# Kernel tuning notes

Hardware: AMD Instinct MI355X
Metric: run time of the kernel (lower is better)

The kernel has to match this reference:

```python
import jax, jax.numpy as jnp
import numpy as np

B, N, M, C, S = 4, 16384, 128, 128, 512  # batch, points, boxes, feat dim, sampled pts


def setup_inputs() -> dict:
    key = jax.random.key(0)
    k1, k2, k3, k4, k5, k6, k7 = jax.random.split(key, 7)
    # point cloud roughly in a LiDAR extent
    xy = jax.random.uniform(k1, (B, N, 2), minval=-50.0, maxval=50.0)
    z = jax.random.uniform(k2, (B, N, 1), minval=-3.0, maxval=3.0)
    points = jnp.concatenate([xy, z], axis=-1).astype(jnp.float32)
    point_features = jax.random.normal(k3, (B, N, C), dtype=jnp.float32)
    # boxes: (cx, cy, cz_bottom, dx, dy, dz, rz)
    ctr_xy = jax.random.uniform(k4, (B, M, 2), minval=-50.0, maxval=50.0)
    ctr_z = jax.random.uniform(k5, (B, M, 1), minval=-3.0, maxval=0.0)
    sizes = jax.random.uniform(k6, (B, M, 3), minval=2.0, maxval=8.0)
    rz = jax.random.uniform(k7, (B, M, 1), minval=-np.pi, maxval=np.pi)
    boxes3d = jnp.concatenate([ctr_xy, ctr_z, sizes, rz], axis=-1).astype(jnp.float32)
    return {"points": points, "point_features": point_features, "boxes3d": boxes3d}


def _pool_one_box(points, feats, box):
    # points (N,3), feats (N,C), box (7,)
    n = points.shape[0]
    cx, cy, cz, dx, dy, dz, rz = box
    cz = cz + 0.5 * dz  # bottom center -> geometric center (mmcv convention)
    sx = points[:, 0] - cx
    sy = points[:, 1] - cy
    cosa = jnp.cos(-rz)
    sina = jnp.sin(-rz)
    lx = sx * cosa - sy * sina
    ly = sx * sina + sy * cosa
    mask = (
        (jnp.abs(points[:, 2] - cz) <= 0.5 * dz)
        & (lx > -0.5 * dx) & (lx < 0.5 * dx)
        & (ly > -0.5 * dy) & (ly < 0.5 * dy)
    )
    cnt = mask.sum(dtype=jnp.int32)
    # rank of each in-box point among in-box points (first-come order)
    rank = jnp.cumsum(mask.astype(jnp.int32)) - 1
    pos = jnp.where(mask, rank, n)  # out-of-range for non-members -> dropped
    table = jnp.zeros((n,), jnp.int32).at[pos].set(
        jnp.arange(n, dtype=jnp.int32), mode="drop")
    # wrap-around duplication when cnt < S (kernel copies k % cnt)
    j = jnp.arange(S, dtype=jnp.int32) % jnp.maximum(cnt, 1)
    idx = table[j]  # (S,)
    pooled = jnp.concatenate([points[idx], feats[idx]], axis=-1)  # (S, 3+C)
    pooled = jnp.where(cnt > 0, pooled, jnp.zeros_like(pooled))
    empty = (cnt == 0).astype(jnp.int32)
    return pooled, empty


def reference(points, point_features, boxes3d):
    # vmap over boxes, then over batch
    per_scene = jax.vmap(_pool_one_box, in_axes=(None, None, 0))
    per_batch = jax.vmap(per_scene, in_axes=(0, 0, 0))
    pooled_features, pooled_empty_flag = per_batch(points, point_features, boxes3d)
    return pooled_features, pooled_empty_flag
```

## Files before the change

### kernel.cpp

```cpp
#include <hip/hip_runtime.h>

#define B_ 4
#define N_ 16384
#define M_ 128
#define C_ 128
#define S_ 512
#define ROW_ 131
#define NCHUNK_ 256
#define TILE_ 128
#define LSTR_ 136
#define KBOX_ 4

typedef float f4_t __attribute__((ext_vector_type(4)));

__device__ __forceinline__ int swz(int j, int col) {
    return j * LSTR_ + (col & 3) * 34 + (col >> 2);
}

__global__ __launch_bounds__(256) void mask_kernel(
    const float* __restrict__ points,
    const float* __restrict__ boxes,
    unsigned long long* __restrict__ masks,
    int* __restrict__ cnts)
{
    const int gwave = blockIdx.x * 4 + (threadIdx.x >> 6);
    const int lane  = threadIdx.x & 63;
    const int grp   = gwave >> 4;
    const int seg   = gwave & 15;
    const int bm0   = grp * KBOX_;
    const int b     = bm0 >> 7;

    const float* pb = points + (size_t)b * N_ * 3;
    float px[16], py[16], pz[16];
    #pragma unroll
    for (int k = 0; k < 16; ++k) {
        const int i = (seg * 16 + k) * 64 + lane;
        px[k] = pb[i*3+0]; py[k] = pb[i*3+1]; pz[k] = pb[i*3+2];
    }

    for (int kb = 0; kb < KBOX_; ++kb) {
        const int bm = bm0 + kb;
        const float* bx = boxes + bm * 7;
        const float cx = bx[0], cy = bx[1], czb = bx[2];
        const float dx = bx[3], dy = bx[4], dzv = bx[5], rz = bx[6];
        const float cz   = __fadd_rn(czb, __fmul_rn(0.5f, dzv));
        const float cosa = (float)cos(-(double)rz);
        const float sina = (float)sin(-(double)rz);
        const float hdx = 0.5f * dx, hdy = 0.5f * dy, hdz = 0.5f * dzv;

        #pragma unroll
        for (int k = 0; k < 16; ++k) {
            const float sx = __fsub_rn(px[k], cx);
            const float sy = __fsub_rn(py[k], cy);
            const float lx = __fsub_rn(__fmul_rn(sx, cosa), __fmul_rn(sy, sina));
            const float ly = __fadd_rn(__fmul_rn(sx, sina), __fmul_rn(sy, cosa));
            const bool pred = (fabsf(__fsub_rn(pz[k], cz)) <= hdz) &&
                              (lx > -hdx) && (lx < hdx) &&
                              (ly > -hdy) && (ly < hdy);
            const unsigned long long m = __ballot(pred);
            if (lane == 0) {
                const int chunk = seg * 16 + k;
                masks[(size_t)bm * NCHUNK_ + chunk] = m;
                cnts [(size_t)bm * NCHUNK_ + chunk] = __popcll(m);
            }
        }
    }
}

__global__ __launch_bounds__(256) void pool_kernel(
    const float* __restrict__ points,
    const float* __restrict__ feats,
    const unsigned long long* __restrict__ masks,
    const int* __restrict__ cnts,
    float* __restrict__ out,
    float* __restrict__ flags_out)
{
    const int bm  = blockIdx.x;
    const int b   = bm >> 7;
    const int tid = threadIdx.x;

    __shared__ int   sc[NCHUNK_];
    __shared__ int   s_idx[S_];
    __shared__ int   jtab[S_ + 1];
    __shared__ float srow[TILE_ * LSTR_];

    const int c = cnts[(size_t)bm * NCHUNK_ + tid];
    sc[tid] = c;
    __syncthreads();
    for (int off = 1; off < NCHUNK_; off <<= 1) {
        const int v = (tid >= off) ? sc[tid - off] : 0;
        __syncthreads();
        sc[tid] += v;
        __syncthreads();
    }
    const int total = sc[NCHUNK_ - 1];
    const int P = sc[tid] - c;

    if (c > 0 && P < S_) {
        unsigned long long m = masks[(size_t)bm * NCHUNK_ + tid];
        int pos = P;
        while (m && pos < S_) {
            const int bit = __ffsll((unsigned long long)m) - 1;
            m &= m - 1;
            s_idx[pos++] = tid * 64 + bit;
        }
    }
    __syncthreads();

    const int cnt_eff = total < S_ ? total : S_;
    const int denom   = cnt_eff > 0 ? cnt_eff : 1;
    for (int s = tid; s <= S_; s += 256) jtab[s] = (s < S_) ? (s % denom) : 0;

    const int T = cnt_eff < TILE_ ? cnt_eff : TILE_;
    if (total == 0) {
        if (tid < LSTR_) srow[tid] = 0.0f;
    } else {
        const int nf4 = T * 32;
        for (int t = tid; t < nf4; t += 256) {
            const int u = t >> 5, q = t & 31;
            const size_t pbase = (size_t)b * N_ + (unsigned)s_idx[u];
            const f4_t v = *(const f4_t*)(feats + pbase * C_ + q * 4);
            #pragma unroll
            for (int jj = 0; jj < 4; ++jj)
                srow[swz(u, 3 + 4 * q + jj)] = v[jj];
        }
        for (int t = tid; t < T * 3; t += 256) {
            const int u = t / 3, k = t - u * 3;
            const size_t pbase = (size_t)b * N_ + (unsigned)s_idx[u];
            srow[swz(u, k)] = points[pbase * 3 + k];
        }
    }
    __syncthreads();

    float* ob = out + (size_t)bm * (S_ * ROW_);
    for (int f = tid; f < (S_ * ROW_) / 4; f += 256) {
        const int e = 4 * f;
        const unsigned s0 = (unsigned)e / (unsigned)ROW_;
        const int col0 = e - (int)s0 * ROW_;
        const int ja = jtab[s0], jb = jtab[s0 + 1];
        f4_t v;
        if ((ja < TILE_) & (jb < TILE_)) {
            #pragma unroll
            for (int jj = 0; jj < 4; ++jj) {
                int col = col0 + jj;
                const bool cross = col >= ROW_;
                col = cross ? col - ROW_ : col;
                const int j = cross ? jb : ja;
                v[jj] = srow[swz(j, col)];
            }
        } else {
            #pragma unroll
            for (int jj = 0; jj < 4; ++jj) {
                int col = col0 + jj;
                unsigned s = s0;
                if (col >= ROW_) { col -= ROW_; ++s; }
                const int j = jtab[s];
                float val;
                if (j < TILE_) {
                    val = srow[swz(j, col)];
                } else {
                    const size_t pbase = (size_t)b * N_ + (unsigned)s_idx[j];
                    val = (col < 3) ? points[pbase * 3 + col]
                                    : feats[pbase * C_ + (col - 3)];
                }
                v[jj] = val;
            }
        }
        __builtin_nontemporal_store(v, (f4_t*)(ob + e));
    }
    if (tid == 0) flags_out[bm] = (total == 0) ? 1.0f : 0.0f;
}

extern "C" void kernel_launch(void* const* d_in, const int* in_sizes, int n_in,
                              void* d_out, int out_size, void* d_ws, size_t ws_size,
                              hipStream_t stream) {
    const float* points = (const float*)d_in[0];
    const float* feats  = (const float*)d_in[1];
    const float* boxes  = (const float*)d_in[2];
    float* out = (float*)d_out;

    unsigned long long* masks = (unsigned long long*)d_ws;
    int* cnts = (int*)((char*)d_ws + (size_t)B_ * M_ * NCHUNK_ * 8);

    float* flags = out + (size_t)B_ * M_ * S_ * ROW_;

    mask_kernel<<<B_ * M_ * 16 / 4 / KBOX_, 256, 0, stream>>>(
        points, boxes, masks, cnts);
    pool_kernel<<<B_ * M_, 256, 0, stream>>>(points, feats, masks, cnts, out, flags);
}
```

Before: 187.2 us.

## Fuse point-in-box mask computation into pooling kernel, keep masks in LDS

Merges the separate mask kernel into the pool kernel. Each block computes its own box's in-box ballot masks and per-chunk counts over all 16384 points, writes them to shared memory, then runs the scan and gather as before. This removes a kernel launch and the global round trip for masks and counts. In exchange, each block now scans the full point array by itself with only 512 blocks of 4 waves, which could lengthen the serial mask phase before the bandwidth-heavy output writes.

```diff
diff --git a/kernel.cpp b/kernel.cpp
--- a/kernel.cpp
+++ b/kernel.cpp
@@ -9,7 +9,6 @@
 #define NCHUNK_ 256
 #define TILE_ 128
 #define LSTR_ 136
-#define KBOX_ 4
 
 typedef float f4_t __attribute__((ext_vector_type(4)));
 
@@ -17,76 +16,55 @@
     return j * LSTR_ + (col & 3) * 34 + (col >> 2);
 }
 
-__global__ __launch_bounds__(256) void mask_kernel(
-    const float* __restrict__ points,
-    const float* __restrict__ boxes,
-    unsigned long long* __restrict__ masks,
-    int* __restrict__ cnts)
-{
-    const int gwave = blockIdx.x * 4 + (threadIdx.x >> 6);
-    const int lane  = threadIdx.x & 63;
-    const int grp   = gwave >> 4;
-    const int seg   = gwave & 15;
-    const int bm0   = grp * KBOX_;
-    const int b     = bm0 >> 7;
-
-    const float* pb = points + (size_t)b * N_ * 3;
-    float px[16], py[16], pz[16];
-    #pragma unroll
-    for (int k = 0; k < 16; ++k) {
-        const int i = (seg * 16 + k) * 64 + lane;
-        px[k] = pb[i*3+0]; py[k] = pb[i*3+1]; pz[k] = pb[i*3+2];
-    }
-
-    for (int kb = 0; kb < KBOX_; ++kb) {
-        const int bm = bm0 + kb;
-        const float* bx = boxes + bm * 7;
-        const float cx = bx[0], cy = bx[1], czb = bx[2];
-        const float dx = bx[3], dy = bx[4], dzv = bx[5], rz = bx[6];
-        const float cz   = __fadd_rn(czb, __fmul_rn(0.5f, dzv));
-        const float cosa = (float)cos(-(double)rz);
-        const float sina = (float)sin(-(double)rz);
-        const float hdx = 0.5f * dx, hdy = 0.5f * dy, hdz = 0.5f * dzv;
-
-        #pragma unroll
-        for (int k = 0; k < 16; ++k) {
-            const float sx = __fsub_rn(px[k], cx);
-            const float sy = __fsub_rn(py[k], cy);
-            const float lx = __fsub_rn(__fmul_rn(sx, cosa), __fmul_rn(sy, sina));
-            const float ly = __fadd_rn(__fmul_rn(sx, sina), __fmul_rn(sy, cosa));
-            const bool pred = (fabsf(__fsub_rn(pz[k], cz)) <= hdz) &&
-                              (lx > -hdx) && (lx < hdx) &&
-                              (ly > -hdy) && (ly < hdy);
-            const unsigned long long m = __ballot(pred);
-            if (lane == 0) {
-                const int chunk = seg * 16 + k;
-                masks[(size_t)bm * NCHUNK_ + chunk] = m;
-                cnts [(size_t)bm * NCHUNK_ + chunk] = __popcll(m);
-            }
-        }
-    }
-}
-
-__global__ __launch_bounds__(256) void pool_kernel(
+__global__ __launch_bounds__(256) void roipool_fused_kernel(
     const float* __restrict__ points,
     const float* __restrict__ feats,
-    const unsigned long long* __restrict__ masks,
-    const int* __restrict__ cnts,
+    const float* __restrict__ boxes,
     float* __restrict__ out,
     float* __restrict__ flags_out)
 {
-    const int bm  = blockIdx.x;
-    const int b   = bm >> 7;
-    const int tid = threadIdx.x;
+    const int bm   = blockIdx.x;
+    const int b    = bm >> 7;
+    const int tid  = threadIdx.x;
+    const int w    = tid >> 6;
+    const int lane = tid & 63;
 
+    __shared__ unsigned long long s_mask[NCHUNK_];
     __shared__ int   sc[NCHUNK_];
     __shared__ int   s_idx[S_];
     __shared__ int   jtab[S_ + 1];
     __shared__ float srow[TILE_ * LSTR_];
 
-    const int c = cnts[(size_t)bm * NCHUNK_ + tid];
-    sc[tid] = c;
+    const float* bx = boxes + bm * 7;
+    const float cx = bx[0], cy = bx[1], czb = bx[2];
+    const float dx = bx[3], dy = bx[4], dzv = bx[5], rz = bx[6];
+    const float cz   = __fadd_rn(czb, __fmul_rn(0.5f, dzv));
+    const float cosa = (float)cos(-(double)rz);
+    const float sina = (float)sin(-(double)rz);
+    const float hdx = 0.5f * dx, hdy = 0.5f * dy, hdz = 0.5f * dzv;
+
+    const float* pb = points + (size_t)b * N_ * 3;
+    #pragma unroll 4
+    for (int k = 0; k < 64; ++k) {
+        const int chunk = w * 64 + k;
+        const int i = chunk * 64 + lane;
+        const float x = pb[i*3+0], y = pb[i*3+1], z = pb[i*3+2];
+        const float sx = __fsub_rn(x, cx);
+        const float sy = __fsub_rn(y, cy);
+        const float lx = __fsub_rn(__fmul_rn(sx, cosa), __fmul_rn(sy, sina));
+        const float ly = __fadd_rn(__fmul_rn(sx, sina), __fmul_rn(sy, cosa));
+        const bool pred = (fabsf(__fsub_rn(z, cz)) <= hdz) &&
+                          (lx > -hdx) && (lx < hdx) &&
+                          (ly > -hdy) && (ly < hdy);
+        const unsigned long long m = __ballot(pred);
+        if (lane == 0) {
+            s_mask[chunk] = m;
+            sc[chunk]     = __popcll(m);
+        }
+    }
     __syncthreads();
+
+    const int c = sc[tid];
     for (int off = 1; off < NCHUNK_; off <<= 1) {
         const int v = (tid >= off) ? sc[tid - off] : 0;
         __syncthreads();
@@ -97,7 +75,7 @@
     const int P = sc[tid] - c;
 
     if (c > 0 && P < S_) {
-        unsigned long long m = masks[(size_t)bm * NCHUNK_ + tid];
+        unsigned long long m = s_mask[tid];
         int pos = P;
         while (m && pos < S_) {
             const int bit = __ffsll((unsigned long long)m) - 1;
@@ -178,13 +156,8 @@
     const float* feats  = (const float*)d_in[1];
     const float* boxes  = (const float*)d_in[2];
     float* out = (float*)d_out;
-
-    unsigned long long* masks = (unsigned long long*)d_ws;
-    int* cnts = (int*)((char*)d_ws + (size_t)B_ * M_ * NCHUNK_ * 8);
-
     float* flags = out + (size_t)B_ * M_ * S_ * ROW_;
 
-    mask_kernel<<<B_ * M_ * 16 / 4 / KBOX_, 256, 0, stream>>>(
-        points, boxes, masks, cnts);
-    pool_kernel<<<B_ * M_, 256, 0, stream>>>(points, feats, masks, cnts, out, flags);
+    roipool_fused_kernel<<<B_ * M_, 256, 0, stream>>>(
+        points, feats, boxes, out, flags);
 }
```

Measured after the change: 205.5 us. +9.8%, slower.
